# Kernel optimization log

Hardware: AMD Instinct MI355X
Metric: run time of the kernel (lower is better)

Reference implementation:

```python
import jax, jax.numpy as jnp
import numpy as np

# Hyperparameters from init_kwargs
M = 32          # number of waveforms / antennas
N = 8192        # code length
T = 1e-3        # logsumexp temperature t
G = 0           # guard zone start
Ewin = N - 1    # guard zone end (E)
W = 0.1         # sidelobe weight


def _groupdiag():
    # Faithful to torch construction for the G == 0 branch:
    # start at (1-W), then overwrite columns [N-E, N-G) and column 0 with W.
    gd = (1.0 - W) * jnp.ones((M * M, N), dtype=jnp.float32)
    gd = gd.at[:, N - Ewin:N - G].set(W)
    gd = gd.at[:, 0:1].set(W)
    return gd


def setup_inputs() -> dict:
    key = jax.random.key(0)
    k1, _ = jax.random.split(key)
    # y_pred[0][:M*N] are normalized phases in [0,1); scaled by 2*pi inside.
    y_pred = jax.random.uniform(k1, (1, M * N), dtype=jnp.float32)
    y_true = jnp.zeros((1,), dtype=jnp.float32)  # unused by the loss
    return {"y_pred": y_pred, "y_true": y_true}


def _loss_and_stats(y_pred):
    x = y_pred[0][: M * N]
    # (N, M) phase matrix, unit-modulus complex waveform
    y = (2.0 * jnp.pi * x).reshape(M, N).T
    y_s = jnp.exp(1j * y)  # complex64, shape (N, M)
    # zero-padded FFT along time: (M, 2N)
    spec = jnp.fft.fft(y_s, n=2 * N, axis=0).T
    # torch: re1[r] = spec[r % M], re2[r] = spec[r // M];
    # sigma[r] = ifft(re1[r] * conj(re2[r]))
    # prod[a, b] = spec[b] * conj(spec[a]) so flattened row r = (a=r//M, b=r%M)
    prod = spec[None, :, :] * jnp.conj(spec)[:, None, :]          # (M, M, 2N)
    sigma = jnp.fft.ifft(prod.reshape(M * M, 2 * N), axis=1)      # (M*M, 2N)
    mag2 = jnp.abs(sigma) ** 2
    # cm[:,0] = |sigma[:,0]|^2 ; cm[:,1:] = |sigma[:,N+1:]|^2
    cm = jnp.concatenate([mag2[:, 0:1], mag2[:, N + 1:]], axis=1)  # (M*M, N)
    cm = cm * _groupdiag()
    idx_eye = np.arange(M) * M + np.arange(M)
    idx_oth = np.array([i * M + j for i in range(M) for j in range(M) if j != i])
    A = cm[idx_eye].T              # (N, M) autocorrelations
    APSL = A[1:].reshape(-1)       # drop zero-lag row
    CPSL = cm[idx_oth].T.reshape(-1)  # cross-correlations
    ac = jnp.concatenate([APSL, CPSL], axis=0) / N / N
    loss = T * jax.nn.logsumexp(ac / T)
    acd = jax.lax.stop_gradient(ac)
    Ad = jax.lax.stop_gradient(APSL)
    Cd = jax.lax.stop_gradient(CPSL)
    stats = (jnp.max(acd), jnp.max(Ad), jnp.max(Cd),
             jnp.sum(acd), jnp.sum(Ad), jnp.sum(Cd))
    return loss, stats


def reference(y_pred, y_true):
    loss, (PSL, APSL_o, CPSL_o, ISL, AISL, CISL) = _loss_and_stats(y_pred)
    return (loss, PSL, APSL_o, CPSL_o, ISL, AISL, CISL)
```

## Files before the change

### kernel.cpp

```cpp
#include <hip/hip_runtime.h>
#include <math.h>

#define M_WAVE 32
#define NLEN 8192
#define FFT_N 16384
#define NPAIR 528

#define TWOPI_F 6.28318530717958647692f

__device__ __forceinline__ float2 cadd(float2 a, float2 b){return make_float2(a.x+b.x, a.y+b.y);}
__device__ __forceinline__ float2 csub(float2 a, float2 b){return make_float2(a.x-b.x, a.y-b.y);}
__device__ __forceinline__ float2 cmul(float2 a, float2 b){return make_float2(a.x*b.x-a.y*b.y, a.x*b.y+a.y*b.x);}
__device__ __forceinline__ float2 mul_i (float2 a){return make_float2(-a.y,  a.x);}
__device__ __forceinline__ float2 mul_mi(float2 a){return make_float2( a.y, -a.x);}

__device__ __forceinline__ unsigned pkc(float2 v){
    unsigned r;
    asm("v_cvt_pk_bf16_f32 %0, %1, %2" : "=v"(r) : "v"(v.x), "v"(v.y));
    return r;
}
__device__ __forceinline__ float2 upkc(unsigned u){
    return make_float2(__uint_as_float(u << 16), __uint_as_float(u & 0xFFFF0000u));
}

__device__ __forceinline__ float2 dpp_xor1(float2 v){
    float2 r;
    r.x = __int_as_float(__builtin_amdgcn_mov_dpp(__float_as_int(v.x), 0xB1, 0xF, 0xF, true));
    r.y = __int_as_float(__builtin_amdgcn_mov_dpp(__float_as_int(v.y), 0xB1, 0xF, 0xF, true));
    return r;
}
__device__ __forceinline__ float2 dpp_xor2(float2 v){
    float2 r;
    r.x = __int_as_float(__builtin_amdgcn_mov_dpp(__float_as_int(v.x), 0x4E, 0xF, 0xF, true));
    r.y = __int_as_float(__builtin_amdgcn_mov_dpp(__float_as_int(v.y), 0x4E, 0xF, 0xF, true));
    return r;
}

__device__ __forceinline__ float waveReduceMax(float v) {
    #pragma unroll
    for (int off = 32; off > 0; off >>= 1) v = fmaxf(v, __shfl_down(v, off, 64));
    return v;
}
__device__ __forceinline__ float waveReduceSum(float v) {
    #pragma unroll
    for (int off = 32; off > 0; off >>= 1) v += __shfl_down(v, off, 64);
    return v;
}

template<int SGN>
__device__ __forceinline__ void dft16_tail(float2 w[16], float2 v[16]){
    const float C1 = 0.923879532511286756f;
    const float S1 = 0.382683432365089772f;
    const float R2 = 0.707106781186547524f;
    const float G = (SGN < 0) ? -1.0f : 1.0f;
    w[5]  = cmul(w[5],  make_float2( C1,  G*S1));
    w[6]  = cmul(w[6],  make_float2( R2,  G*R2));
    w[7]  = cmul(w[7],  make_float2( S1,  G*C1));
    w[9]  = cmul(w[9],  make_float2( R2,  G*R2));
    w[10] = (SGN<0) ? mul_mi(w[10]) : mul_i(w[10]);
    w[11] = cmul(w[11], make_float2(-R2,  G*R2));
    w[13] = cmul(w[13], make_float2( S1,  G*C1));
    w[14] = cmul(w[14], make_float2(-R2,  G*R2));
    w[15] = cmul(w[15], make_float2(-C1, -G*S1));
    #pragma unroll
    for (int k0 = 0; k0 < 4; ++k0){
        float2 a = w[k0*4+0], b = w[k0*4+1], c = w[k0*4+2], d = w[k0*4+3];
        float2 t0 = cadd(a,c), t1 = csub(a,c), t2 = cadd(b,d), t3 = csub(b,d);
        float2 j3 = (SGN < 0) ? mul_mi(t3) : mul_i(t3);
        v[k0]    = cadd(t0,t2);
        v[k0+4]  = cadd(t1,j3);
        v[k0+8]  = csub(t0,t2);
        v[k0+12] = csub(t1,j3);
    }
}

template<int SGN>
__device__ __forceinline__ void dft16(float2 v[16]){
    float2 w[16];
    #pragma unroll
    for (int n0 = 0; n0 < 4; ++n0){
        float2 a = v[n0], b = v[n0+4], c = v[n0+8], d = v[n0+12];
        float2 t0 = cadd(a,c), t1 = csub(a,c), t2 = cadd(b,d), t3 = csub(b,d);
        float2 j3 = (SGN < 0) ? mul_mi(t3) : mul_i(t3);
        w[n0]    = cadd(t0,t2);
        w[4+n0]  = cadd(t1,j3);
        w[8+n0]  = csub(t0,t2);
        w[12+n0] = csub(t1,j3);
    }
    dft16_tail<SGN>(w, v);
}

__device__ __forceinline__ void dft16_zero8(float2 v[16]){
    float2 w[16];
    #pragma unroll
    for (int n0 = 0; n0 < 4; ++n0){
        float2 a = v[n0], b = v[n0+4];
        w[n0]    = cadd(a,b);
        w[4+n0]  = make_float2(a.x + b.y, a.y - b.x);
        w[8+n0]  = csub(a,b);
        w[12+n0] = make_float2(a.x - b.y, a.y + b.x);
    }
    dft16_tail<-1>(w, v);
}

template<int SGN>
__device__ __forceinline__ void dft16_ip(float2 v[16]){
    const float C1 = 0.923879532511286756f;
    const float S1 = 0.382683432365089772f;
    const float R2 = 0.707106781186547524f;
    const float G = (SGN < 0) ? -1.0f : 1.0f;
    #pragma unroll
    for (int n1 = 0; n1 < 4; ++n1){
        float2 a = v[n1], b = v[n1+4], c = v[n1+8], d = v[n1+12];
        float2 t0 = cadd(a,c), t1 = csub(a,c), t2 = cadd(b,d), t3 = csub(b,d);
        float2 j3 = (SGN < 0) ? mul_mi(t3) : mul_i(t3);
        v[n1]    = cadd(t0,t2);
        v[n1+4]  = cadd(t1,j3);
        v[n1+8]  = csub(t0,t2);
        v[n1+12] = csub(t1,j3);
    }
    v[5]  = cmul(v[5],  make_float2( C1,  G*S1));
    v[6]  = cmul(v[6],  make_float2( R2,  G*R2));
    v[7]  = cmul(v[7],  make_float2( S1,  G*C1));
    v[9]  = cmul(v[9],  make_float2( R2,  G*R2));
    v[10] = (SGN<0) ? mul_mi(v[10]) : mul_i(v[10]);
    v[11] = cmul(v[11], make_float2(-R2,  G*R2));
    v[13] = cmul(v[13], make_float2( S1,  G*C1));
    v[14] = cmul(v[14], make_float2(-R2,  G*R2));
    v[15] = cmul(v[15], make_float2(-C1, -G*S1));
    #pragma unroll
    for (int kl = 0; kl < 4; ++kl){
        float2 a = v[4*kl], b = v[4*kl+1], c = v[4*kl+2], d = v[4*kl+3];
        float2 t0 = cadd(a,c), t1 = csub(a,c), t2 = cadd(b,d), t3 = csub(b,d);
        float2 j3 = (SGN < 0) ? mul_mi(t3) : mul_i(t3);
        v[4*kl]   = cadd(t0,t2);
        v[4*kl+1] = cadd(t1,j3);
        v[4*kl+2] = csub(t0,t2);
        v[4*kl+3] = csub(t1,j3);
    }
}

template<int SGN>
__device__ __forceinline__ void twchain16(float2 v[16], float theta){
    float th = (SGN < 0) ? -theta : theta;
    float s1,c1; __sincosf(th, &s1, &c1);
    float s4,c4; __sincosf(4.0f*th, &s4, &c4);
    float2 w1 = make_float2(c1,s1), w4 = make_float2(c4,s4);
    float2 lo2 = cmul(w1,w1), lo3 = cmul(lo2,w1);
    float2 hi2 = cmul(w4,w4), hi3 = cmul(hi2,w4);
    float2 lo[4] = {make_float2(1.f,0.f), w1, lo2, lo3};
    float2 hi[4] = {make_float2(1.f,0.f), w4, hi2, hi3};
    #pragma unroll
    for (int s = 1; s < 16; ++s){
        v[s] = cmul(v[s], cmul(hi[s>>2], lo[s&3]));
    }
}

__device__ __forceinline__ int L1swz(int e){
    return (e & ~63) | (((e & 63) + ((e >> 6) & 15)) & 63);
}

__global__ __launch_bounds__(512, 2) void fwd_fft_kernel(const float* __restrict__ x,
                                                         unsigned* __restrict__ spec) {
    __shared__ float2 X8[8192];
    const int bx = blockIdx.x, m = bx >> 1, hf = bx & 1;
    const int tid = threadIdx.x;

    #pragma unroll 1
    for (int cc = 0; cc < 2; ++cc){
        const int j = cc*512 + tid;
        float2 v[16];
        #pragma unroll
        for (int s = 0; s < 8; ++s){
            float ph = TWOPI_F * x[m*NLEN + s*1024 + j];
            float sn,cs; __sincosf(ph,&sn,&cs);
            v[s] = make_float2(cs,sn);
        }
        dft16_zero8(v);
        const float th = TWOPI_F * (float)j / 16384.0f;
        float sb,cb; __sincosf(-(float)(8*hf)*th, &sb, &cb);
        float ss,cs2; __sincosf(-th, &ss, &cs2);
        float2 wcur = make_float2(cb,sb), wstep = make_float2(cs2,ss);
        #pragma unroll
        for (int d = 0; d < 8; ++d){
            X8[d*1024 + L1swz(j)] = cmul(v[8*hf + d], wcur);
            wcur = cmul(wcur, wstep);
        }
    }
    __syncthreads();

    const int wv = tid >> 6, jB = tid & 63;
    float2 v[16];
    #pragma unroll
    for (int t = 0; t < 16; ++t) v[t] = X8[wv*1024 + t*64 + ((jB + t) & 63)];
    dft16<-1>(v);
    twchain16<-1>(v, TWOPI_F * (float)jB / 1024.0f);
    #pragma unroll
    for (int sp = 0; sp < 16; ++sp) X8[wv*1024 + sp*64 + ((jB + 4*sp) & 63)] = v[sp];

    {
        const int bl = (tid & 63) >> 2, jC = tid & 3;
        #pragma unroll
        for (int a = 0; a < 16; ++a)
            v[a] = X8[wv*1024 + bl*64 + ((4*a + jC + 4*bl) & 63)];
        dft16<-1>(v);
        twchain16<-1>(v, TWOPI_F * (float)jC / 64.0f);
        const bool odd1 = (jC & 1) != 0;
        const bool odd2 = (jC & 2) != 0;
        #pragma unroll
        for (int e = 0; e < 16; ++e){
            float2 p = dpp_xor2(v[e]);
            float2 t = odd2 ? csub(p, v[e]) : cadd(v[e], p);
            float2 q = dpp_xor1(t);
            float2 re = odd1 ? csub(q, t) : cadd(t, q);
            float2 ro = odd1 ? cadd(q, mul_i(t)) : cadd(t, mul_mi(q));
            v[e] = odd2 ? ro : re;
        }
        const int u = ((jC & 1) << 1) | (jC >> 1);
        uint4* dst = (uint4*)(spec + (size_t)m*FFT_N + (8*hf + wv)*1024 + bl*64 + u*16);
        #pragma unroll
        for (int e = 0; e < 4; ++e)
            dst[e] = make_uint4(pkc(v[4*e]), pkc(v[4*e+1]), pkc(v[4*e+2]), pkc(v[4*e+3]));
    }
}

__global__ __launch_bounds__(512, 4) void pair_kernel(const unsigned* __restrict__ spec,
                                                      float4* __restrict__ rec) {
    __shared__ unsigned X[FFT_N];
    const int r = blockIdx.x, tid = threadIdx.x;
    const bool is_auto = (r >= 496);
    int a, b, rec_idx;
    if (is_auto){
        a = b = r - 496;
        rec_idx = r - 496;
    } else {
        int t = r; a = 0; int rem = M_WAVE - 1;
        while (t >= rem){ t -= rem; ++a; rem = M_WAVE - 1 - a; }
        b = a + 1 + t;
        rec_idx = M_WAVE + r;
    }
    const int jC = tid & 3;
    const int u = ((jC & 1) << 1) | (jC >> 1);
    const bool odd1 = (jC & 1) != 0;
    const bool odd2 = (jC & 2) != 0;

    #pragma unroll
    for (int p = 0; p < 2; ++p){
        const int blk = (tid >> 2) + 128*p;
        float2 v[16];
        const uint4* pa = (const uint4*)(spec + (size_t)a*FFT_N + blk*64 + u*16);
        const uint4* pb = (const uint4*)(spec + (size_t)b*FFT_N + blk*64 + u*16);
        #pragma unroll
        for (int e = 0; e < 4; ++e){
            uint4 A = pa[e], B = pb[e];
            float2 a0 = upkc(A.x), a1 = upkc(A.y), a2 = upkc(A.z), a3 = upkc(A.w);
            float2 b0 = upkc(B.x), b1 = upkc(B.y), b2 = upkc(B.z), b3 = upkc(B.w);
            v[4*e+0] = make_float2(b0.x*a0.x + b0.y*a0.y, b0.y*a0.x - b0.x*a0.y);
            v[4*e+1] = make_float2(b1.x*a1.x + b1.y*a1.y, b1.y*a1.x - b1.x*a1.y);
            v[4*e+2] = make_float2(b2.x*a2.x + b2.y*a2.y, b2.y*a2.x - b2.x*a2.y);
            v[4*e+3] = make_float2(b3.x*a3.x + b3.y*a3.y, b3.y*a3.x - b3.x*a3.y);
        }
        #pragma unroll
        for (int e = 0; e < 16; ++e){
            float2 q = dpp_xor1(v[e]);
            float2 t = odd1 ? csub(q, v[e]) : cadd(v[e], q);
            float2 pp = dpp_xor2(t);
            float2 re = odd2 ? csub(pp, t) : cadd(t, pp);
            float2 ro = odd2 ? csub(pp, mul_i(t)) : cadd(t, mul_i(pp));
            v[e] = odd1 ? ro : re;
        }
        twchain16<+1>(v, TWOPI_F * (float)jC / 64.0f);
        dft16_ip<+1>(v);
        const int rot = 4*(blk & 15);
        #pragma unroll
        for (int s = 0; s < 16; ++s){
            const int t = 4*(s&3) + (s>>2);
            X[blk*64 + ((4*t + jC + rot) & 63)] = pkc(v[s]);
        }
    }
    const int wv = tid >> 6, jB = tid & 63;
    #pragma unroll
    for (int p = 0; p < 2; ++p){
        const int sB = wv + 8*p;
        float2 v[16];
        #pragma unroll
        for (int sp = 0; sp < 16; ++sp) v[sp] = upkc(X[sB*1024 + sp*64 + ((jB + 4*sp) & 63)]);
        twchain16<+1>(v, TWOPI_F * (float)jB / 1024.0f);
        dft16_ip<+1>(v);
        #pragma unroll
        for (int s = 0; s < 16; ++s){
            const int t = 4*(s&3) + (s>>2);
            X[sB*1024 + t*64 + ((jB + t) & 63)] = pkc(v[s]);
        }
    }
    __syncthreads();

    const float CSCALE = 0.1f / (16384.0f * 16384.0f);
    float uval[2][16];
    float lm = 0.f, lsum = 0.f;
    #pragma unroll
    for (int p = 0; p < 2; ++p){
        const int tp = tid + 512*p;
        const int baseA = L1swz(tp);
        float2 v[16];
        #pragma unroll
        for (int s = 0; s < 16; ++s) v[s] = upkc(X[s*1024 + baseA]);
        twchain16<+1>(v, TWOPI_F * (float)tp / 16384.0f);
        dft16_ip<+1>(v);
        const bool j0 = (tp == 0);
        #pragma unroll
        for (int s = 0; s < 16; ++s){
            const int t = 4*(s&3) + (s>>2);
            float uu = CSCALE * (v[s].x*v[s].x + v[s].y*v[s].y);
            uval[p][s] = uu;
            if (is_auto){
                bool valid = (t > 8) || ((t == 8) && !j0);
                if (valid){ lm = fmaxf(lm, uu); lsum += uu; }
            } else {
                bool inv = (t == 8) && j0;
                if (!inv){ lm = fmaxf(lm, uu); lsum += uu; }
                if (t == 0 && j0) lsum += uu;
            }
        }
    }
    __syncthreads();

    float* scratch = (float*)X;
    const int lane = tid & 63, wvv = tid >> 6;
    float wm = waveReduceMax(lm);
    float wsm = waveReduceSum(lsum);
    if (lane == 0){ scratch[wvv] = wm; scratch[8+wvv] = wsm; }
    __syncthreads();
    float m_b = scratch[0], sumu = scratch[8];
    #pragma unroll
    for (int i = 1; i < 8; ++i){ m_b = fmaxf(m_b, scratch[i]); sumu += scratch[8+i]; }

    const float invTN2 = 1.0f / 67108.864f;
    float le = 0.f;
    #pragma unroll
    for (int p = 0; p < 2; ++p){
        const bool j0 = (p == 0) && (tid == 0);
        #pragma unroll
        for (int s = 0; s < 16; ++s){
            const int t = 4*(s&3) + (s>>2);
            float ex = __expf((uval[p][s] - m_b) * invTN2);
            if (is_auto){
                bool valid = (t > 8) || ((t == 8) && !j0);
                if (valid) le += ex;
            } else {
                bool inv = (t == 8) && j0;
                if (!inv) le += ((t == 0 && j0) ? 2.f : 1.f) * ex;
            }
        }
    }
    float wle = waveReduceSum(le);
    if (lane == 0) scratch[16+wvv] = wle;
    __syncthreads();
    if (tid == 0){
        float sb2 = 0.f;
        #pragma unroll
        for (int i = 0; i < 8; ++i) sb2 += scratch[16+i];
        rec[rec_idx] = make_float4(m_b, sumu, sb2, 0.f);
    }
}

__global__ __launch_bounds__(64) void final_kernel(const float4* __restrict__ rec,
                                                   float* __restrict__ out) {
    const int lane = threadIdx.x;
    float mA = 0.f, mC = 0.f;
    for (int r = lane; r < NPAIR; r += 64){
        float mx = rec[r].x;
        if (r < M_WAVE) mA = fmaxf(mA, mx); else mC = fmaxf(mC, mx);
    }
    #pragma unroll
    for (int off = 32; off > 0; off >>= 1){
        mA = fmaxf(mA, __shfl_xor(mA, off, 64));
        mC = fmaxf(mC, __shfl_xor(mC, off, 64));
    }
    const float Mall = fmaxf(mA, mC);
    const float invTN2f = 1.0f / 67108.864f;
    double S = 0.0, sA = 0.0, sC = 0.0;
    for (int r = lane; r < NPAIR; r += 64){
        float4 rv = rec[r];
        S += (double)rv.z * (double)__expf((rv.x - Mall)*invTN2f);
        if (r < M_WAVE) sA += (double)rv.y; else sC += (double)rv.y;
    }
    #pragma unroll
    for (int off = 32; off > 0; off >>= 1){
        S  += __shfl_xor(S,  off, 64);
        sA += __shfl_xor(sA, off, 64);
        sC += __shfl_xor(sC, off, 64);
    }
    if (lane == 0){
        const double invN2 = 1.0/67108864.0;
        out[0] = (float)((double)Mall*invN2 + 1e-3*log(S));
        out[1] = (float)((double)Mall*invN2);
        out[2] = mA;
        out[3] = mC;
        out[4] = (float)((sA + sC)*invN2);
        out[5] = (float)sA;
        out[6] = (float)sC;
    }
}

extern "C" void kernel_launch(void* const* d_in, const int* in_sizes, int n_in,
                              void* d_out, int out_size, void* d_ws, size_t ws_size,
                              hipStream_t stream) {
    (void)in_sizes; (void)n_in; (void)out_size; (void)ws_size;
    const float* x = (const float*)d_in[0];
    float* out = (float*)d_out;

    unsigned* spec = (unsigned*)d_ws;
    float4* rec = (float4*)((char*)d_ws + (size_t)M_WAVE * FFT_N * sizeof(unsigned));

    fwd_fft_kernel<<<64, 512, 0, stream>>>(x, spec);
    pair_kernel<<<NPAIR, 512, 0, stream>>>(spec, rec);
    final_kernel<<<1, 64, 0, stream>>>(rec, out);
}
```

Measured before the change: 56.17 us.

## Pack two autocorrelation spectra into one complex IFFT per block

```diff
diff --git a/kernel.cpp b/kernel.cpp
--- a/kernel.cpp
+++ b/kernel.cpp
@@ -227,17 +227,16 @@
 __global__ __launch_bounds__(512, 4) void pair_kernel(const unsigned* __restrict__ spec,
                                                       float4* __restrict__ rec) {
     __shared__ unsigned X[FFT_N];
+    __shared__ float scr2[64];
     const int r = blockIdx.x, tid = threadIdx.x;
-    const bool is_auto = (r >= 496);
-    int a, b, rec_idx;
-    if (is_auto){
-        a = b = r - 496;
-        rec_idx = r - 496;
+    const bool is_packed = (r >= 496);
+    int a, b;
+    if (is_packed){
+        const int k = r - 496; a = 2*k; b = 2*k + 1;
     } else {
         int t = r; a = 0; int rem = M_WAVE - 1;
         while (t >= rem){ t -= rem; ++a; rem = M_WAVE - 1 - a; }
         b = a + 1 + t;
-        rec_idx = M_WAVE + r;
     }
     const int jC = tid & 3;
     const int u = ((jC & 1) << 1) | (jC >> 1);
@@ -255,10 +254,17 @@
             uint4 A = pa[e], B = pb[e];
             float2 a0 = upkc(A.x), a1 = upkc(A.y), a2 = upkc(A.z), a3 = upkc(A.w);
             float2 b0 = upkc(B.x), b1 = upkc(B.y), b2 = upkc(B.z), b3 = upkc(B.w);
-            v[4*e+0] = make_float2(b0.x*a0.x + b0.y*a0.y, b0.y*a0.x - b0.x*a0.y);
-            v[4*e+1] = make_float2(b1.x*a1.x + b1.y*a1.y, b1.y*a1.x - b1.x*a1.y);
-            v[4*e+2] = make_float2(b2.x*a2.x + b2.y*a2.y, b2.y*a2.x - b2.x*a2.y);
-            v[4*e+3] = make_float2(b3.x*a3.x + b3.y*a3.y, b3.y*a3.x - b3.x*a3.y);
+            if (is_packed){
+                v[4*e+0] = make_float2(a0.x*a0.x + a0.y*a0.y, b0.x*b0.x + b0.y*b0.y);
+                v[4*e+1] = make_float2(a1.x*a1.x + a1.y*a1.y, b1.x*b1.x + b1.y*b1.y);
+                v[4*e+2] = make_float2(a2.x*a2.x + a2.y*a2.y, b2.x*b2.x + b2.y*b2.y);
+                v[4*e+3] = make_float2(a3.x*a3.x + a3.y*a3.y, b3.x*b3.x + b3.y*b3.y);
+            } else {
+                v[4*e+0] = make_float2(b0.x*a0.x + b0.y*a0.y, b0.y*a0.x - b0.x*a0.y);
+                v[4*e+1] = make_float2(b1.x*a1.x + b1.y*a1.y, b1.y*a1.x - b1.x*a1.y);
+                v[4*e+2] = make_float2(b2.x*a2.x + b2.y*a2.y, b2.y*a2.x - b2.x*a2.y);
+                v[4*e+3] = make_float2(b3.x*a3.x + b3.y*a3.y, b3.y*a3.x - b3.x*a3.y);
+            }
         }
         #pragma unroll
         for (int e = 0; e < 16; ++e){
@@ -296,71 +302,151 @@
     __syncthreads();
 
     const float CSCALE = 0.1f / (16384.0f * 16384.0f);
-    float uval[2][16];
-    float lm = 0.f, lsum = 0.f;
-    #pragma unroll
-    for (int p = 0; p < 2; ++p){
-        const int tp = tid + 512*p;
-        const int baseA = L1swz(tp);
-        float2 v[16];
-        #pragma unroll
-        for (int s = 0; s < 16; ++s) v[s] = upkc(X[s*1024 + baseA]);
-        twchain16<+1>(v, TWOPI_F * (float)tp / 16384.0f);
-        dft16_ip<+1>(v);
-        const bool j0 = (tp == 0);
-        #pragma unroll
-        for (int s = 0; s < 16; ++s){
-            const int t = 4*(s&3) + (s>>2);
-            float uu = CSCALE * (v[s].x*v[s].x + v[s].y*v[s].y);
-            uval[p][s] = uu;
-            if (is_auto){
-                bool valid = (t > 8) || ((t == 8) && !j0);
-                if (valid){ lm = fmaxf(lm, uu); lsum += uu; }
-            } else {
+    const float invTN2 = 1.0f / 67108.864f;
+    const int lane = tid & 63, wvv = tid >> 6;
+
+    if (!is_packed){
+        float uval[2][16];
+        float lm = 0.f, lsum = 0.f;
+        #pragma unroll
+        for (int p = 0; p < 2; ++p){
+            const int tp = tid + 512*p;
+            const int baseA = L1swz(tp);
+            float2 v[16];
+            #pragma unroll
+            for (int s = 0; s < 16; ++s) v[s] = upkc(X[s*1024 + baseA]);
+            twchain16<+1>(v, TWOPI_F * (float)tp / 16384.0f);
+            dft16_ip<+1>(v);
+            const bool j0 = (tp == 0);
+            #pragma unroll
+            for (int s = 0; s < 16; ++s){
+                const int t = 4*(s&3) + (s>>2);
+                float uu = CSCALE * (v[s].x*v[s].x + v[s].y*v[s].y);
+                uval[p][s] = uu;
                 bool inv = (t == 8) && j0;
                 if (!inv){ lm = fmaxf(lm, uu); lsum += uu; }
                 if (t == 0 && j0) lsum += uu;
             }
         }
-    }
-    __syncthreads();
-
-    float* scratch = (float*)X;
-    const int lane = tid & 63, wvv = tid >> 6;
-    float wm = waveReduceMax(lm);
-    float wsm = waveReduceSum(lsum);
-    if (lane == 0){ scratch[wvv] = wm; scratch[8+wvv] = wsm; }
-    __syncthreads();
-    float m_b = scratch[0], sumu = scratch[8];
-    #pragma unroll
-    for (int i = 1; i < 8; ++i){ m_b = fmaxf(m_b, scratch[i]); sumu += scratch[8+i]; }
-
-    const float invTN2 = 1.0f / 67108.864f;
-    float le = 0.f;
-    #pragma unroll
-    for (int p = 0; p < 2; ++p){
-        const bool j0 = (p == 0) && (tid == 0);
-        #pragma unroll
-        for (int s = 0; s < 16; ++s){
-            const int t = 4*(s&3) + (s>>2);
-            float ex = __expf((uval[p][s] - m_b) * invTN2);
-            if (is_auto){
-                bool valid = (t > 8) || ((t == 8) && !j0);
-                if (valid) le += ex;
-            } else {
+        __syncthreads();
+
+        float* scratch = (float*)X;
+        float wm = waveReduceMax(lm);
+        float wsm = waveReduceSum(lsum);
+        if (lane == 0){ scratch[wvv] = wm; scratch[8+wvv] = wsm; }
+        __syncthreads();
+        float m_b = scratch[0], sumu = scratch[8];
+        #pragma unroll
+        for (int i = 1; i < 8; ++i){ m_b = fmaxf(m_b, scratch[i]); sumu += scratch[8+i]; }
+
+        float le = 0.f;
+        #pragma unroll
+        for (int p = 0; p < 2; ++p){
+            const bool j0 = (p == 0) && (tid == 0);
+            #pragma unroll
+            for (int s = 0; s < 16; ++s){
+                const int t = 4*(s&3) + (s>>2);
+                float ex = __expf((uval[p][s] - m_b) * invTN2);
                 bool inv = (t == 8) && j0;
                 if (!inv) le += ((t == 0 && j0) ? 2.f : 1.f) * ex;
             }
         }
-    }
-    float wle = waveReduceSum(le);
-    if (lane == 0) scratch[16+wvv] = wle;
-    __syncthreads();
-    if (tid == 0){
-        float sb2 = 0.f;
-        #pragma unroll
-        for (int i = 0; i < 8; ++i) sb2 += scratch[16+i];
-        rec[rec_idx] = make_float4(m_b, sumu, sb2, 0.f);
+        float wle = waveReduceSum(le);
+        if (lane == 0) scratch[16+wvv] = wle;
+        __syncthreads();
+        if (tid == 0){
+            float sb2 = 0.f;
+            #pragma unroll
+            for (int i = 0; i < 8; ++i) sb2 += scratch[16+i];
+            rec[M_WAVE + r] = make_float4(m_b, sumu, sb2, 0.f);
+        }
+    } else {
+        unsigned zpk[2][16];
+        #pragma unroll
+        for (int p = 0; p < 2; ++p){
+            const int tp = tid + 512*p;
+            const int baseA = L1swz(tp);
+            float2 v[16];
+            #pragma unroll
+            for (int s = 0; s < 16; ++s) v[s] = upkc(X[s*1024 + baseA]);
+            twchain16<+1>(v, TWOPI_F * (float)tp / 16384.0f);
+            dft16_ip<+1>(v);
+            #pragma unroll
+            for (int s = 0; s < 16; ++s) zpk[p][s] = pkc(v[s]);
+        }
+        __syncthreads();
+        #pragma unroll
+        for (int p = 0; p < 2; ++p){
+            const int tp = tid + 512*p;
+            #pragma unroll
+            for (int s = 0; s < 16; ++s){
+                const int t = 4*(s&3) + (s>>2);
+                X[t*1024 + tp] = zpk[p][s];
+            }
+        }
+        __syncthreads();
+
+        float lma = 0.f, lmb = 0.f, lsa = 0.f, lsb = 0.f;
+        #pragma unroll
+        for (int p = 0; p < 2; ++p){
+            const int tp = tid + 512*p;
+            #pragma unroll
+            for (int s = 0; s < 16; ++s){
+                const int t = 4*(s&3) + (s>>2);
+                if (t < 8) continue;
+                if (t == 8 && tp == 0) continue;
+                const int n = t*1024 + tp;
+                float2 z  = upkc(X[n]);
+                float2 zc = upkc(X[FFT_N - n]);
+                float ar = 0.5f*(z.x + zc.x), ai = 0.5f*(z.y - zc.y);
+                float br = 0.5f*(z.x - zc.x), bi = 0.5f*(z.y + zc.y);
+                float ua = CSCALE*(ar*ar + ai*ai);
+                float ub = CSCALE*(br*br + bi*bi);
+                lma = fmaxf(lma, ua); lsa += ua;
+                lmb = fmaxf(lmb, ub); lsb += ub;
+            }
+        }
+        float wma = waveReduceMax(lma), wmb = waveReduceMax(lmb);
+        float wsa = waveReduceSum(lsa), wsb = waveReduceSum(lsb);
+        if (lane == 0){ scr2[wvv]=wma; scr2[8+wvv]=wmb; scr2[16+wvv]=wsa; scr2[24+wvv]=wsb; }
+        __syncthreads();
+        float m_a = scr2[0], m_b = scr2[8], s_a = scr2[16], s_b = scr2[24];
+        #pragma unroll
+        for (int i = 1; i < 8; ++i){
+            m_a = fmaxf(m_a, scr2[i]);    m_b = fmaxf(m_b, scr2[8+i]);
+            s_a += scr2[16+i];            s_b += scr2[24+i];
+        }
+        float lea = 0.f, leb = 0.f;
+        #pragma unroll
+        for (int p = 0; p < 2; ++p){
+            const int tp = tid + 512*p;
+            #pragma unroll
+            for (int s = 0; s < 16; ++s){
+                const int t = 4*(s&3) + (s>>2);
+                if (t < 8) continue;
+                if (t == 8 && tp == 0) continue;
+                const int n = t*1024 + tp;
+                float2 z  = upkc(X[n]);
+                float2 zc = upkc(X[FFT_N - n]);
+                float ar = 0.5f*(z.x + zc.x), ai = 0.5f*(z.y - zc.y);
+                float br = 0.5f*(z.x - zc.x), bi = 0.5f*(z.y + zc.y);
+                float ua = CSCALE*(ar*ar + ai*ai);
+                float ub = CSCALE*(br*br + bi*bi);
+                lea += __expf((ua - m_a)*invTN2);
+                leb += __expf((ub - m_b)*invTN2);
+            }
+        }
+        float wlea = waveReduceSum(lea), wleb = waveReduceSum(leb);
+        if (lane == 0){ scr2[32+wvv] = wlea; scr2[40+wvv] = wleb; }
+        __syncthreads();
+        if (tid == 0){
+            float ta = 0.f, tb = 0.f;
+            #pragma unroll
+            for (int i = 0; i < 8; ++i){ ta += scr2[32+i]; tb += scr2[40+i]; }
+            const int k = r - 496;
+            rec[2*k]   = make_float4(m_a, s_a, ta, 0.f);
+            rec[2*k+1] = make_float4(m_b, s_b, tb, 0.f);
+        }
     }
 }
 
@@ -414,6 +500,6 @@
     float4* rec = (float4*)((char*)d_ws + (size_t)M_WAVE * FFT_N * sizeof(unsigned));
 
     fwd_fft_kernel<<<64, 512, 0, stream>>>(x, spec);
-    pair_kernel<<<NPAIR, 512, 0, stream>>>(spec, rec);
+    pair_kernel<<<512, 512, 0, stream>>>(spec, rec);
     final_kernel<<<1, 64, 0, stream>>>(rec, out);
 }
```

Measured after the change: 52.18 us. -7.1%, faster.
